# Kernel tuning notes

Hardware: AMD Instinct MI355X
Metric: run time of the kernel (lower is better)

The kernel has to match this reference:

```python
import jax, jax.numpy as jnp
import numpy as np

BETA = 0.25


def setup_inputs() -> dict:
    key = jax.random.key(0)
    k1, k2 = jax.random.split(key)
    B, D, H, W, K = 16, 256, 32, 32, 8192
    z_e = jax.random.normal(k1, (B, D, H, W), dtype=jnp.float32)
    # codebook init uniform(-1/K, 1/K) as in torch
    codebook = jax.random.uniform(k2, (K, D), dtype=jnp.float32,
                                  minval=-1.0 / K, maxval=1.0 / K)
    return {"z_e": z_e, "codebook": codebook}


def reference(z_e, codebook):
    B, D, H, W = z_e.shape
    K = codebook.shape[0]
    # (B, D, H, W) -> (BHW, D)
    z_flat = jnp.transpose(z_e, (0, 2, 3, 1)).reshape(-1, D)

    # distances computed under no_grad in torch -> stop_gradient here
    zf = jax.lax.stop_gradient(z_flat)
    cb = jax.lax.stop_gradient(codebook)
    # ||z||^2 + ||e||^2 - 2 z.e  -> (BHW, K)
    dist = ((zf * zf).sum(axis=1, keepdims=True)
            + (cb * cb).sum(axis=1)[None, :]
            - 2.0 * (zf @ cb.T))
    indices = jnp.argmin(dist, axis=1)  # (BHW,)

    # embedding gather, reshape back to (B, D, H, W)
    z_q_flat = codebook[indices]
    z_q = jnp.transpose(z_q_flat.reshape(B, H, W, D), (0, 3, 1, 2))

    # straight-through estimator
    z_q_st = z_e + jax.lax.stop_gradient(z_q - z_e)

    codebook_loss = jnp.mean((jax.lax.stop_gradient(z_q) - z_e) ** 2)
    commitment_loss = jnp.mean((z_q - jax.lax.stop_gradient(z_e)) ** 2)
    vq_loss = codebook_loss + BETA * commitment_loss

    # perplexity: one_hot(indices).mean(0) == counts / N
    N = z_flat.shape[0]
    counts = jnp.zeros((K,), dtype=z_flat.dtype).at[indices].add(1.0)
    avg_probs = counts / N
    perplexity = jnp.exp(-jnp.sum(avg_probs * jnp.log(avg_probs + 1e-10)))

    return (z_q_st, vq_loss, indices.reshape(B, H, W), perplexity)
```

## Files before the change

### kernel.cpp

```cpp
#include <hip/hip_runtime.h>

#define DD 256
#define KK 8192
#define HW 1024
#define NROWS 16384
#define NELEM 4194304
#define MT 32
#define MARGIN 6e-4f
#define WCAP 512
#define NT 256
#define NSLICE 4

typedef __attribute__((ext_vector_type(8))) short short8;
typedef __attribute__((ext_vector_type(4))) float f32x4;
typedef unsigned short ushort;
typedef unsigned int uint;
typedef unsigned long long u64;

__device__ __forceinline__ float np_pw128_sq(const float* p) {
  float r[8];
#pragma unroll
  for (int j = 0; j < 8; ++j) r[j] = __fmul_rn(p[j], p[j]);
  for (int i = 8; i < 128; i += 8) {
#pragma unroll
    for (int j = 0; j < 8; ++j)
      r[j] = __fadd_rn(r[j], __fmul_rn(p[i + j], p[i + j]));
  }
  return __fadd_rn(__fadd_rn(__fadd_rn(r[0], r[1]), __fadd_rn(r[2], r[3])),
                   __fadd_rn(__fadd_rn(r[4], r[5]), __fadd_rn(r[6], r[7])));
}

__device__ __forceinline__ ushort f2bf(float x) {
  uint u = __float_as_uint(x);
  u += 0x7FFF + ((u >> 16) & 1);
  return (ushort)(u >> 16);
}

struct Top2 { float m1, m2; int i1; };

__device__ __forceinline__ void top2_upd(Top2& s, const f32x4 a,
                                         const f32x4 Bs, int ibase) {
  float d0 = fmaf(-2.f, a[0], Bs[0]);
  float d1 = fmaf(-2.f, a[1], Bs[1]);
  float d2 = fmaf(-2.f, a[2], Bs[2]);
  float d3 = fmaf(-2.f, a[3], Bs[3]);
  float lo01 = fminf(d0, d1), hi01 = fmaxf(d0, d1);
  int io01 = d1 < d0 ? ibase + 1 : ibase;
  float lo23 = fminf(d2, d3), hi23 = fmaxf(d2, d3);
  int io23 = d3 < d2 ? ibase + 3 : ibase + 2;
  float n1 = fminf(lo01, lo23);
  int ni = lo23 < lo01 ? io23 : io01;
  float n2 = fminf(fmaxf(lo01, lo23), fminf(hi01, hi23));
  s.m2 = fminf(fmaxf(s.m1, n1), fminf(s.m2, n2));
  s.i1 = n1 < s.m1 ? ni : s.i1;
  s.m1 = fminf(s.m1, n1);
}

__device__ __forceinline__ void top2_bfly(Top2& s, int off) {
  float om1 = __shfl_xor(s.m1, off);
  int oi1 = __shfl_xor(s.i1, off);
  float om2 = __shfl_xor(s.m2, off);
  s.m2 = fminf(fmaxf(s.m1, om1), fminf(s.m2, om2));
  s.i1 = om1 < s.m1 ? oi1 : s.i1;
  s.m1 = fminf(s.m1, om1);
}

__device__ __forceinline__ uint pack_m2(float m2, int i1) {
  uint u = __float_as_uint(m2);
  uint hi = u & 0xFFFF0000u;
  if ((u & 0x80000000u) && (u & 0xFFFFu)) hi += 0x10000u;
  return hi | (uint)i1;
}

__global__ __launch_bounds__(256) void vq_prep(const float* __restrict__ cb,
                                               float* __restrict__ Bk,
                                               ushort* __restrict__ cbB) {
  const int b = blockIdx.x, t = threadIdx.x;
  if (b < 32) {
    int k = b * 256 + t;
    const float* p = cb + (size_t)k * DD;
    Bk[k] = __fadd_rn(np_pw128_sq(p), np_pw128_sq(p + 128));
  } else {
    int tid = (b - 32) * 256 + t;
    int g = tid >> 9, s = (tid >> 6) & 7, lane = tid & 63;
    int code = g * 16 + (lane & 15);
    int dbase = s * 32 + (lane >> 4) * 8;
    const float* p = cb + (size_t)code * DD + dbase;
    ushort bb[8];
#pragma unroll
    for (int j = 0; j < 8; ++j) bb[j] = f2bf(p[j]);
    uint4 pk;
    pk.x = bb[0] | ((uint)bb[1] << 16);
    pk.y = bb[2] | ((uint)bb[3] << 16);
    pk.z = bb[4] | ((uint)bb[5] << 16);
    pk.w = bb[6] | ((uint)bb[7] << 16);
    *(uint4*)(cbB + (size_t)tid * 8) = pk;
  }
}

__global__ __launch_bounds__(256) void vq_screen(
    const float* __restrict__ z, const ushort* __restrict__ cbB,
    const float* __restrict__ Bk, float* __restrict__ tA,
    uint* __restrict__ tB) {
  __shared__ ushort ztB[MT][264];
  __shared__ float BkS[2048];
  const int bid = blockIdx.x;
  const int rt = bid >> 2, cs = bid & 3;
  const int t = threadIdx.x;
  const int n0 = rt * MT;
  const int bimg = n0 >> 10, hw0 = n0 & 1023;
  const float* zb = z + (size_t)bimg * DD * HW + hw0;

  for (int li = t; li < MT * 128; li += 256) {
    int r = li & 31, dp = li >> 5;
    float v0 = zb[(size_t)(2 * dp) * HW + r];
    float v1 = zb[(size_t)(2 * dp + 1) * HW + r];
    *(uint*)&ztB[r][2 * dp] = (uint)f2bf(v0) | ((uint)f2bf(v1) << 16);
  }
  for (int li = t; li < 2048; li += 256)
    BkS[li] = Bk[cs * 2048 + li];
  __syncthreads();

  const int w = t >> 6, lane = t & 63;
  const int quad = lane >> 4, n16 = lane & 15;

  short8 aF[2][8];
#pragma unroll
  for (int rg = 0; rg < 2; ++rg)
#pragma unroll
    for (int s = 0; s < 8; ++s)
      aF[rg][s] = *(const short8*)&ztB[rg * 16 + n16][s * 32 + quad * 8];

  const int gg0 = cs * 128 + w * 32;
  const int cbase = cs * 2048;
  Top2 c0 = {3.4e38f, 3.4e38f, 0}, c1 = {3.4e38f, 3.4e38f, 0};

  short8 b0[8], b1[8];
  {
    const ushort* bp = cbB + (size_t)gg0 * 4096 + lane * 8;
#pragma unroll
    for (int s = 0; s < 8; ++s) b0[s] = *(const short8*)(bp + s * 512);
  }

  for (int gp = 0; gp < 16; ++gp) {
    const int gg = gg0 + gp * 2;
    {
      const ushort* bp = cbB + (size_t)(gg + 1) * 4096 + lane * 8;
#pragma unroll
      for (int s = 0; s < 8; ++s) b1[s] = *(const short8*)(bp + s * 512);
    }
    {
      f32x4 a0 = {0.f, 0.f, 0.f, 0.f}, a1 = {0.f, 0.f, 0.f, 0.f};
#pragma unroll
      for (int s = 0; s < 8; ++s) {
        a0 = __builtin_amdgcn_mfma_f32_16x16x32_bf16(b0[s], aF[0][s], a0, 0, 0, 0);
        a1 = __builtin_amdgcn_mfma_f32_16x16x32_bf16(b0[s], aF[1][s], a1, 0, 0, 0);
      }
      const f32x4 Bs = *(const f32x4*)(BkS + gg * 16 - cbase + quad * 4);
      top2_upd(c0, a0, Bs, quad * 4);
      top2_upd(c1, a1, Bs, quad * 4);
    }
    if (gp < 15) {
      const ushort* bp = cbB + (size_t)(gg + 2) * 4096 + lane * 8;
#pragma unroll
      for (int s = 0; s < 8; ++s) b0[s] = *(const short8*)(bp + s * 512);
    }
    {
      f32x4 a0 = {0.f, 0.f, 0.f, 0.f}, a1 = {0.f, 0.f, 0.f, 0.f};
#pragma unroll
      for (int s = 0; s < 8; ++s) {
        a0 = __builtin_amdgcn_mfma_f32_16x16x32_bf16(b1[s], aF[0][s], a0, 0, 0, 0);
        a1 = __builtin_amdgcn_mfma_f32_16x16x32_bf16(b1[s], aF[1][s], a1, 0, 0, 0);
      }
      const f32x4 Bs = *(const f32x4*)(BkS + (gg + 1) * 16 - cbase + quad * 4);
      top2_upd(c0, a0, Bs, 16 + quad * 4);
      top2_upd(c1, a1, Bs, 16 + quad * 4);
    }
    top2_bfly(c0, 16); top2_bfly(c0, 32);
    top2_bfly(c1, 16); top2_bfly(c1, 32);
    const size_t tbase = (size_t)(gg >> 1) * NROWS + n0;
    if (quad == 0) {
      tA[tbase + n16] = c0.m1;
      tB[tbase + n16] = pack_m2(c0.m2, c0.i1);
    } else if (quad == 1) {
      tA[tbase + 16 + n16] = c1.m1;
      tB[tbase + 16 + n16] = pack_m2(c1.m2, c1.i1);
    }
    c0.m1 = 3.4e38f; c0.m2 = 3.4e38f; c0.i1 = 0;
    c1.m1 = 3.4e38f; c1.m2 = 3.4e38f; c1.i1 = 0;
  }
}

__global__ __launch_bounds__(256) void vq_rerank(
    const float* __restrict__ z, const float* __restrict__ cb,
    const float* __restrict__ Bk, const float* __restrict__ tA,
    const uint* __restrict__ tB, float* __restrict__ out,
    int* __restrict__ hist, float* __restrict__ loss_acc,
    u64* __restrict__ rowBest) {
  __shared__ float zt[MT][DD + 1];
  __shared__ float thr[MT];
  __shared__ float ArS[MT];
  __shared__ float partial[4][MT];
  __shared__ int wl[WCAP];
  __shared__ int wcnt;
  __shared__ int kwin[MT];
  __shared__ float lred[4];

  const int t = threadIdx.x;
  const int n0 = blockIdx.x * MT;
  const int bimg = n0 >> 10, hw0 = n0 & 1023;
  const float* zb = z + (size_t)bimg * DD * HW + hw0;

  if (t == 0) wcnt = 0;
  for (int li = t; li < MT * DD; li += 256) {
    int d = li >> 5, r = li & 31;
    zt[r][d] = zb[d * HW + r];
  }

  const int w = t >> 6, lane = t & 63;
  const int r = t & 31, j = t >> 5;

  float mn = 3.4e38f;
#pragma unroll 4
  for (int k = 0; k < 32; ++k)
    mn = fminf(mn, tA[(size_t)(j * 32 + k) * NROWS + n0 + r]);
  mn = fminf(mn, __shfl_xor(mn, 32));
  if (lane < 32) partial[w][r] = mn;
  __syncthreads();
  if (t < MT) {
    thr[t] = fminf(fminf(partial[0][t], partial[1][t]),
                   fminf(partial[2][t], partial[3][t])) + MARGIN;
  } else if (t >= 128 && t < 192) {
    int rr = (t - 128) >> 1, half = t & 1;
    float h = np_pw128_sq(&zt[rr][half * 128]);
    float ho = __shfl_xor(h, 1);
    if (half == 0) ArS[rr] = __fadd_rn(h, ho);
  }
  __syncthreads();

  auto exact_one = [&](int rr, int code) {
    const float* cp = cb + (size_t)code * DD;
    float dot = 0.f;
#pragma unroll
    for (int d0 = 0; d0 < DD; d0 += 4) {
      float4 v = *(const float4*)(cp + d0);
      dot = fmaf(zt[rr][d0 + 0], v.x, dot);
      dot = fmaf(zt[rr][d0 + 1], v.y, dot);
      dot = fmaf(zt[rr][d0 + 2], v.z, dot);
      dot = fmaf(zt[rr][d0 + 3], v.w, dot);
    }
    float bd = __fsub_rn(__fadd_rn(ArS[rr], Bk[code]), __fmul_rn(2.f, dot));
    atomicMin(&rowBest[n0 + rr],
              ((u64)__float_as_uint(bd) << 32) | (unsigned)code);
  };

  const float th = thr[r];
  for (int k = 0; k < 32; ++k) {
    const int tile = j * 32 + k;
    const float a = tA[(size_t)tile * NROWS + n0 + r];
    if (a <= th) {
      const uint pk = tB[(size_t)tile * NROWS + n0 + r];
      const float m2f = __uint_as_float(pk & 0xFFFF0000u);
      if (m2f <= th) {
        for (int c = 0; c < 32; ++c) {
          int pos = atomicAdd(&wcnt, 1);
          if (pos < WCAP) wl[pos] = (r << 16) | (tile * 32 + c);
          else exact_one(r, tile * 32 + c);
        }
      } else {
        int pos = atomicAdd(&wcnt, 1);
        if (pos < WCAP) wl[pos] = (r << 16) | (tile * 32 + (int)(pk & 31u));
        else exact_one(r, tile * 32 + (int)(pk & 31u));
      }
    }
  }
  __syncthreads();

  const int cnt = min(wcnt, WCAP);
  for (int e = t; e < cnt; e += 256) {
    const int ent = wl[e];
    exact_one(ent >> 16, ent & 0xFFFF);
  }
  __syncthreads();

  if (t < MT) {
    u64 key = atomicMin(&rowBest[n0 + t], 0xFFFFFFFFFFFFFFFFull);
    int bi = (int)(key & 0xFFFFFFFFull);
    kwin[t] = bi;
    atomicAdd(&hist[bi], 1);
    out[(size_t)NELEM + 1 + n0 + t] = (float)bi;
  }
  __syncthreads();

  float lsum = 0.f;
  for (int it = 0; it < MT * DD / 256; ++it) {
    int li = it * 256 + t;
    int d = li >> 5, rr = li & 31;
    float ze = zt[rr][d];
    float zq = cb[(size_t)kwin[rr] * DD + d];
    float diff = __fsub_rn(zq, ze);
    float st = __fadd_rn(ze, diff);
    out[(size_t)(bimg * DD + d) * HW + hw0 + rr] = st;
    lsum = fmaf(diff, diff, lsum);
  }
#pragma unroll
  for (int off = 32; off > 0; off >>= 1) lsum += __shfl_down(lsum, off);
  if (lane == 0) lred[w] = lsum;
  __syncthreads();
  if (t == 0)
    atomicAdd(loss_acc, ((lred[0] + lred[1]) + (lred[2] + lred[3])));
}

__global__ __launch_bounds__(256) void vq_final(const int* __restrict__ hist,
                                                const float* __restrict__ loss,
                                                float* __restrict__ out) {
  __shared__ float sred[256];
  int t = threadIdx.x;
  float s = 0.f;
  for (int k = t; k < KK; k += 256) {
    float p = (float)hist[k] * (1.f / 16384.f);
    s += p * logf(p + 1e-10f);
  }
  sred[t] = s;
  __syncthreads();
  for (int off = 128; off > 0; off >>= 1) {
    if (t < off) sred[t] += sred[t + off];
    __syncthreads();
  }
  if (t == 0) {
    float L = loss[0] / (float)NELEM;
    out[NELEM] = 1.25f * L;
    out[(size_t)NELEM + 1 + NROWS] = expf(-sred[0]);
  }
}

extern "C" void kernel_launch(void* const* d_in, const int* in_sizes, int n_in,
                              void* d_out, int out_size, void* d_ws, size_t ws_size,
                              hipStream_t stream) {
  const float* z = (const float*)d_in[0];
  const float* cb = (const float*)d_in[1];
  float* out = (float*)d_out;

  float* wsf = (float*)d_ws;
  int* hist = (int*)d_ws;
  float* loss = wsf + 8192;
  float* Bk = wsf + 8448;
  u64* rowBest = (u64*)(wsf + 16640);
  ushort* cbB = (ushort*)(wsf + 49408);
  float* tA = wsf + 1097984;
  uint* tB = (uint*)(wsf + 5292288);

  hipMemsetAsync(d_ws, 0, 8448 * sizeof(float), stream);
  hipMemsetAsync(rowBest, 0xFF, NROWS * sizeof(u64), stream);
  vq_prep<<<1056, 256, 0, stream>>>(cb, Bk, cbB);
  vq_screen<<<(NROWS / MT) * NSLICE, 256, 0, stream>>>(z, cbB, Bk, tA, tB);
  vq_rerank<<<NROWS / MT, 256, 0, stream>>>(z, cb, Bk, tA, tB, out,
                                            hist, loss, rowBest);
  vq_final<<<1, 256, 0, stream>>>(hist, loss, out);
}
```

Baseline: 241.1 us.

## Widen screen row tile to 64 and compute per-row min via atomics

The screening kernel now processes 64 rows per block instead of 32, reusing each loaded bf16 codebook fragment across four MFMA row groups and halving the codebook traffic per row. It also tracks each row's minimum screened distance and publishes it with an order-preserving uint atomicMin. The rerank kernel then reads that value directly instead of scanning all 256 tA partial minima per row. This costs more registers for the extra A fragments and accumulators, which may lower occupancy, and adds global atomics plus a larger memset and workspace reshuffle.

```diff
diff --git a/kernel.cpp b/kernel.cpp
--- a/kernel.cpp
+++ b/kernel.cpp
@@ -6,9 +6,9 @@
 #define NROWS 16384
 #define NELEM 4194304
 #define MT 32
+#define MS 64
 #define MARGIN 6e-4f
-#define WCAP 512
-#define NT 256
+#define WCAP 1024
 #define NSLICE 4
 
 typedef __attribute__((ext_vector_type(8))) short short8;
@@ -34,6 +34,14 @@
   uint u = __float_as_uint(x);
   u += 0x7FFF + ((u >> 16) & 1);
   return (ushort)(u >> 16);
+}
+
+__device__ __forceinline__ uint fenc(float f) {
+  uint u = __float_as_uint(f);
+  return (u & 0x80000000u) ? ~u : (u | 0x80000000u);
+}
+__device__ __forceinline__ float fdec(uint k) {
+  return __uint_as_float((k & 0x80000000u) ? (k & 0x7FFFFFFFu) : ~k);
 }
 
 struct Top2 { float m1, m2; int i1; };
@@ -98,42 +106,60 @@
   }
 }
 
+#define GG_BODY(BUF, GGI, IB)                                                  \
+  {                                                                            \
+    f32x4 A0 = {0,0,0,0}, A1 = {0,0,0,0}, A2 = {0,0,0,0}, A3 = {0,0,0,0};      \
+    _Pragma("unroll")                                                          \
+    for (int s = 0; s < 8; ++s) {                                              \
+      A0 = __builtin_amdgcn_mfma_f32_16x16x32_bf16(BUF[s], aF0[s], A0, 0, 0, 0);\
+      A1 = __builtin_amdgcn_mfma_f32_16x16x32_bf16(BUF[s], aF1[s], A1, 0, 0, 0);\
+      A2 = __builtin_amdgcn_mfma_f32_16x16x32_bf16(BUF[s], aF2[s], A2, 0, 0, 0);\
+      A3 = __builtin_amdgcn_mfma_f32_16x16x32_bf16(BUF[s], aF3[s], A3, 0, 0, 0);\
+    }                                                                          \
+    const f32x4 Bs = *(const f32x4*)(BkS + (GGI) * 16 - cbase + quad * 4);     \
+    top2_upd(c0, A0, Bs, IB); top2_upd(c1, A1, Bs, IB);                        \
+    top2_upd(c2, A2, Bs, IB); top2_upd(c3, A3, Bs, IB);                        \
+  }
+
 __global__ __launch_bounds__(256) void vq_screen(
     const float* __restrict__ z, const ushort* __restrict__ cbB,
     const float* __restrict__ Bk, float* __restrict__ tA,
-    uint* __restrict__ tB) {
-  __shared__ ushort ztB[MT][264];
+    uint* __restrict__ tB, uint* __restrict__ rowMinG) {
+  __shared__ ushort ztB[MS][264];
   __shared__ float BkS[2048];
   const int bid = blockIdx.x;
   const int rt = bid >> 2, cs = bid & 3;
   const int t = threadIdx.x;
-  const int n0 = rt * MT;
+  const int n0 = rt * MS;
   const int bimg = n0 >> 10, hw0 = n0 & 1023;
   const float* zb = z + (size_t)bimg * DD * HW + hw0;
 
-  for (int li = t; li < MT * 128; li += 256) {
-    int r = li & 31, dp = li >> 5;
+  for (int li = t; li < MS * 128; li += 256) {
+    int r = li & 63, dp = li >> 6;
     float v0 = zb[(size_t)(2 * dp) * HW + r];
     float v1 = zb[(size_t)(2 * dp + 1) * HW + r];
     *(uint*)&ztB[r][2 * dp] = (uint)f2bf(v0) | ((uint)f2bf(v1) << 16);
   }
-  for (int li = t; li < 2048; li += 256)
-    BkS[li] = Bk[cs * 2048 + li];
+  for (int li = t; li < 2048; li += 256) BkS[li] = Bk[cs * 2048 + li];
   __syncthreads();
 
   const int w = t >> 6, lane = t & 63;
   const int quad = lane >> 4, n16 = lane & 15;
 
-  short8 aF[2][8];
-#pragma unroll
-  for (int rg = 0; rg < 2; ++rg)
-#pragma unroll
-    for (int s = 0; s < 8; ++s)
-      aF[rg][s] = *(const short8*)&ztB[rg * 16 + n16][s * 32 + quad * 8];
+  short8 aF0[8], aF1[8], aF2[8], aF3[8];
+#pragma unroll
+  for (int s = 0; s < 8; ++s) {
+    aF0[s] = *(const short8*)&ztB[n16][s * 32 + quad * 8];
+    aF1[s] = *(const short8*)&ztB[16 + n16][s * 32 + quad * 8];
+    aF2[s] = *(const short8*)&ztB[32 + n16][s * 32 + quad * 8];
+    aF3[s] = *(const short8*)&ztB[48 + n16][s * 32 + quad * 8];
+  }
 
   const int gg0 = cs * 128 + w * 32;
   const int cbase = cs * 2048;
   Top2 c0 = {3.4e38f, 3.4e38f, 0}, c1 = {3.4e38f, 3.4e38f, 0};
+  Top2 c2 = {3.4e38f, 3.4e38f, 0}, c3 = {3.4e38f, 3.4e38f, 0};
+  float rmin = 3.4e38f;
 
   short8 b0[8], b1[8];
   {
@@ -149,58 +175,46 @@
 #pragma unroll
       for (int s = 0; s < 8; ++s) b1[s] = *(const short8*)(bp + s * 512);
     }
-    {
-      f32x4 a0 = {0.f, 0.f, 0.f, 0.f}, a1 = {0.f, 0.f, 0.f, 0.f};
-#pragma unroll
-      for (int s = 0; s < 8; ++s) {
-        a0 = __builtin_amdgcn_mfma_f32_16x16x32_bf16(b0[s], aF[0][s], a0, 0, 0, 0);
-        a1 = __builtin_amdgcn_mfma_f32_16x16x32_bf16(b0[s], aF[1][s], a1, 0, 0, 0);
-      }
-      const f32x4 Bs = *(const f32x4*)(BkS + gg * 16 - cbase + quad * 4);
-      top2_upd(c0, a0, Bs, quad * 4);
-      top2_upd(c1, a1, Bs, quad * 4);
-    }
+    GG_BODY(b0, gg, quad * 4)
     if (gp < 15) {
       const ushort* bp = cbB + (size_t)(gg + 2) * 4096 + lane * 8;
 #pragma unroll
       for (int s = 0; s < 8; ++s) b0[s] = *(const short8*)(bp + s * 512);
     }
-    {
-      f32x4 a0 = {0.f, 0.f, 0.f, 0.f}, a1 = {0.f, 0.f, 0.f, 0.f};
-#pragma unroll
-      for (int s = 0; s < 8; ++s) {
-        a0 = __builtin_amdgcn_mfma_f32_16x16x32_bf16(b1[s], aF[0][s], a0, 0, 0, 0);
-        a1 = __builtin_amdgcn_mfma_f32_16x16x32_bf16(b1[s], aF[1][s], a1, 0, 0, 0);
-      }
-      const f32x4 Bs = *(const f32x4*)(BkS + (gg + 1) * 16 - cbase + quad * 4);
-      top2_upd(c0, a0, Bs, 16 + quad * 4);
-      top2_upd(c1, a1, Bs, 16 + quad * 4);
-    }
+    GG_BODY(b1, gg + 1, 16 + quad * 4)
     top2_bfly(c0, 16); top2_bfly(c0, 32);
     top2_bfly(c1, 16); top2_bfly(c1, 32);
+    top2_bfly(c2, 16); top2_bfly(c2, 32);
+    top2_bfly(c3, 16); top2_bfly(c3, 32);
     const size_t tbase = (size_t)(gg >> 1) * NROWS + n0;
     if (quad == 0) {
-      tA[tbase + n16] = c0.m1;
-      tB[tbase + n16] = pack_m2(c0.m2, c0.i1);
+      tA[tbase + n16] = c0.m1; tB[tbase + n16] = pack_m2(c0.m2, c0.i1);
+      rmin = fminf(rmin, c0.m1);
     } else if (quad == 1) {
-      tA[tbase + 16 + n16] = c1.m1;
-      tB[tbase + 16 + n16] = pack_m2(c1.m2, c1.i1);
-    }
-    c0.m1 = 3.4e38f; c0.m2 = 3.4e38f; c0.i1 = 0;
-    c1.m1 = 3.4e38f; c1.m2 = 3.4e38f; c1.i1 = 0;
-  }
+      tA[tbase + 16 + n16] = c1.m1; tB[tbase + 16 + n16] = pack_m2(c1.m2, c1.i1);
+      rmin = fminf(rmin, c1.m1);
+    } else if (quad == 2) {
+      tA[tbase + 32 + n16] = c2.m1; tB[tbase + 32 + n16] = pack_m2(c2.m2, c2.i1);
+      rmin = fminf(rmin, c2.m1);
+    } else {
+      tA[tbase + 48 + n16] = c3.m1; tB[tbase + 48 + n16] = pack_m2(c3.m2, c3.i1);
+      rmin = fminf(rmin, c3.m1);
+    }
+    c0 = Top2{3.4e38f, 3.4e38f, 0}; c1 = Top2{3.4e38f, 3.4e38f, 0};
+    c2 = Top2{3.4e38f, 3.4e38f, 0}; c3 = Top2{3.4e38f, 3.4e38f, 0};
+  }
+  atomicMin(&rowMinG[n0 + quad * 16 + n16], fenc(rmin));
 }
 
 __global__ __launch_bounds__(256) void vq_rerank(
     const float* __restrict__ z, const float* __restrict__ cb,
     const float* __restrict__ Bk, const float* __restrict__ tA,
-    const uint* __restrict__ tB, float* __restrict__ out,
-    int* __restrict__ hist, float* __restrict__ loss_acc,
-    u64* __restrict__ rowBest) {
+    const uint* __restrict__ tB, const uint* __restrict__ rowMinG,
+    float* __restrict__ out, int* __restrict__ hist,
+    float* __restrict__ loss_acc, u64* __restrict__ rowBest) {
   __shared__ float zt[MT][DD + 1];
   __shared__ float thr[MT];
   __shared__ float ArS[MT];
-  __shared__ float partial[4][MT];
   __shared__ int wl[WCAP];
   __shared__ int wcnt;
   __shared__ int kwin[MT];
@@ -216,20 +230,13 @@
     int d = li >> 5, r = li & 31;
     zt[r][d] = zb[d * HW + r];
   }
+  __syncthreads();
 
   const int w = t >> 6, lane = t & 63;
   const int r = t & 31, j = t >> 5;
 
-  float mn = 3.4e38f;
-#pragma unroll 4
-  for (int k = 0; k < 32; ++k)
-    mn = fminf(mn, tA[(size_t)(j * 32 + k) * NROWS + n0 + r]);
-  mn = fminf(mn, __shfl_xor(mn, 32));
-  if (lane < 32) partial[w][r] = mn;
-  __syncthreads();
   if (t < MT) {
-    thr[t] = fminf(fminf(partial[0][t], partial[1][t]),
-                   fminf(partial[2][t], partial[3][t])) + MARGIN;
+    thr[t] = fdec(rowMinG[n0 + t]) + MARGIN;
   } else if (t >= 128 && t < 192) {
     int rr = (t - 128) >> 1, half = t & 1;
     float h = np_pw128_sq(&zt[rr][half * 128]);
@@ -345,16 +352,18 @@
   int* hist = (int*)d_ws;
   float* loss = wsf + 8192;
   float* Bk = wsf + 8448;
-  u64* rowBest = (u64*)(wsf + 16640);
-  ushort* cbB = (ushort*)(wsf + 49408);
-  float* tA = wsf + 1097984;
-  uint* tB = (uint*)(wsf + 5292288);
+  uint* rowMinG = (uint*)(wsf + 16640);
+  u64* rowBest = (u64*)(wsf + 33024);
+  ushort* cbB = (ushort*)(wsf + 65792);
+  float* tA = wsf + 1114368;
+  uint* tB = (uint*)(wsf + 5308672);
 
   hipMemsetAsync(d_ws, 0, 8448 * sizeof(float), stream);
-  hipMemsetAsync(rowBest, 0xFF, NROWS * sizeof(u64), stream);
+  hipMemsetAsync(wsf + 16640, 0xFF, 196608, stream);
   vq_prep<<<1056, 256, 0, stream>>>(cb, Bk, cbB);
-  vq_screen<<<(NROWS / MT) * NSLICE, 256, 0, stream>>>(z, cbB, Bk, tA, tB);
-  vq_rerank<<<NROWS / MT, 256, 0, stream>>>(z, cb, Bk, tA, tB, out,
+  vq_screen<<<(NROWS / MS) * NSLICE, 256, 0, stream>>>(z, cbB, Bk, tA, tB,
+                                                       rowMinG);
+  vq_rerank<<<NROWS / MT, 256, 0, stream>>>(z, cb, Bk, tA, tB, rowMinG, out,
                                             hist, loss, rowBest);
   vq_final<<<1, 256, 0, stream>>>(hist, loss, out);
 }
```

Measured after the change: 228.7 us. 5.2% less time.
